# Optimization experiments

Measured on AMD Instinct MI355X. Metric: run time of the kernel, lower is better.

The kernel has to match this reference:

```python
import jax, jax.numpy as jnp
import numpy as np


def _lstm_scan(x_tm, W, b, reset_tm=None):
    """Run an hk.LSTM-equivalent scan over time-major x_tm [L, B, D].

    Gate order i, g, f, o with +1 forget-gate bias (haiku convention).
    If reset_tm [L, B] (bool) is given, state is zeroed BEFORE the step
    whenever reset is True (hk.ResetCore semantics).
    """
    B = x_tm.shape[1]
    H = b.shape[0] // 4

    def step(carry, inp):
        h, c = carry
        if reset_tm is None:
            xt = inp
        else:
            xt, rt = inp
            keep = jnp.logical_not(rt)[:, None]
            h = jnp.where(keep, h, 0.0)
            c = jnp.where(keep, c, 0.0)
        gates = jnp.concatenate([xt, h], axis=-1) @ W + b  # [B, 4H]
        i, g, f, o = jnp.split(gates, 4, axis=-1)
        c = jax.nn.sigmoid(f + 1.0) * c + jax.nn.sigmoid(i) * jnp.tanh(g)
        h = jax.nn.sigmoid(o) * jnp.tanh(c)
        return (h, c), h

    init = (jnp.zeros((B, H), x_tm.dtype), jnp.zeros((B, H), x_tm.dtype))
    xs = x_tm if reset_tm is None else (x_tm, reset_tm)
    _, hs = jax.lax.scan(step, init, xs)
    return hs  # [L, B, H]


def setup_inputs() -> dict:
    key = jax.random.key(0)
    kx, kwf, kwb, kl = jax.random.split(key, 4)
    B, L, D, H = 32, 1024, 512, 512
    scale = 1.0 / np.sqrt(D + H)
    return {
        "x": jax.random.normal(kx, (B, L, D), dtype=jnp.float32),
        "W_fwd": jax.random.normal(kwf, (D + H, 4 * H), dtype=jnp.float32) * scale,
        "b_fwd": jnp.zeros((4 * H,), dtype=jnp.float32),
        "W_bwd": jax.random.normal(kwb, (D + H, 4 * H), dtype=jnp.float32) * scale,
        "b_bwd": jnp.zeros((4 * H,), dtype=jnp.float32),
        "lengths": jax.random.randint(kl, (B,), 1, L + 1),
    }


def reference(x, W_fwd, b_fwd, W_bwd, b_bwd, lengths):
    B, L, D = x.shape
    # reset mask: True for t >= length - 1 (as in original module)
    mask = jnp.arange(L)[None, :] >= lengths[:, None] - 1  # [B, L]

    # forward direction
    h_f = _lstm_scan(jnp.swapaxes(x, 0, 1), W_fwd, b_fwd)  # [L, B, H]
    h_f = jnp.swapaxes(h_f, 0, 1)  # [B, L, H]

    # backward direction: flip time, run ResetCore LSTM, flip back
    x_b = jnp.flip(x, axis=1)
    mask_b = jnp.flip(mask, axis=1)
    h_b = _lstm_scan(jnp.swapaxes(x_b, 0, 1), W_bwd, b_bwd,
                     jnp.swapaxes(mask_b, 0, 1))  # [L, B, H]
    h_b = jnp.flip(jnp.swapaxes(h_b, 0, 1), axis=1)  # [B, L, H]

    return jnp.concatenate([h_f, h_b], axis=-1)  # [B, L, 2H]
```

## Files before the change

### kernel.cpp

```cpp
#include <hip/hip_runtime.h>
#include <stdint.h>


typedef __attribute__((ext_vector_type(8))) short  short8;
typedef __attribute__((ext_vector_type(4))) float  floatx4;

#define LSEQ 1024
#define NB   32
#define DD   512
#define HH   512
#define NG   2048

#define WX_OFF  0ul
#define WH_OFF  (4ul<<20)
#define X_OFF   (8ul<<20)
#define H_OFF   (40ul<<20)
#define RST_OFF ((40ul<<20)+(384ul<<10))
#define TAG_OFF ((40ul<<20)+(388ul<<10))
#define Z_OFF   (41ul<<20)
#define ZF_BYTES (2ul*LSEQ*NB*NG*4)
#define ZB_BYTES (2ul*LSEQ*NB*NG*2)
#define WS_NEED_F32 (Z_OFF + ZF_BYTES)
#define WS_NEED_B16 (Z_OFF + ZB_BYTES)

__device__ inline uint16_t f2bf(float f) {
  uint32_t u = __float_as_uint(f);
  u += 0x7fff + ((u >> 16) & 1);
  return (uint16_t)(u >> 16);
}
__device__ inline float fsigm(float x) { return 1.0f / (1.0f + __expf(-x)); }
__device__ inline float ftanh(float x) { return 1.0f - 2.0f / (__expf(2.0f * x) + 1.0f); }

template <typename ZT> __device__ inline void zstore(ZT* p, float v);
template <> __device__ inline void zstore<float>(float* p, float v) { *p = v; }
template <> __device__ inline void zstore<uint16_t>(uint16_t* p, float v) { *p = f2bf(v); }

template <typename ZT> __device__ inline float2 zld2(const ZT* p);
template <> __device__ inline float2 zld2<float>(const float* p) { return *(const float2*)p; }
template <> __device__ inline float2 zld2<uint16_t>(const uint16_t* p) {
  uint32_t u = *(const uint32_t*)p;
  float2 r;
  r.x = __uint_as_float((u & 0xffffu) << 16);
  r.y = __uint_as_float(u & 0xffff0000u);
  return r;
}

__global__ void k_init(const int* __restrict__ len, uint32_t* __restrict__ rst,
                       int* __restrict__ tags, uint16_t* __restrict__ H)
{
  int tid = blockIdx.x * blockDim.x + threadIdx.x;
  int stride = gridDim.x * blockDim.x;
  for (int i = tid; i < 512; i += stride) tags[i] = 0;
  for (int i = tid; i < 2 * 2 * NB * HH; i += stride) H[i] = 0;
  for (int t = tid; t < LSEQ; t += stride) {
    uint32_t m = 0;
    for (int b = 0; b < NB; ++b)
      m |= ((uint32_t)(t <= LSEQ - len[b])) << b;
    rst[t] = m;
  }
}

__global__ void k_wcast(const float* __restrict__ Wf, const float* __restrict__ Wb,
                        uint16_t* __restrict__ WX, uint16_t* __restrict__ WH)
{
  int tid = blockIdx.x * blockDim.x + threadIdx.x;
  if (tid >= 2 * 1024 * 512) return;
  int dir = tid >> 19;
  int r = tid & ((1 << 19) - 1);
  int k = r >> 9;
  int n4 = (r & 511) * 4;
  const float* W = dir ? Wb : Wf;
  const float4 v = *(const float4*)(W + (size_t)k * NG + n4);
  uint16_t* dst;
  int kk;
  if (k < DD) { dst = WX + (size_t)dir * NG * DD; kk = k; }
  else        { dst = WH + (size_t)dir * NG * HH; kk = k - DD; }
  dst[(size_t)(n4 + 0) * 512 + kk] = f2bf(v.x);
  dst[(size_t)(n4 + 1) * 512 + kk] = f2bf(v.y);
  dst[(size_t)(n4 + 2) * 512 + kk] = f2bf(v.z);
  dst[(size_t)(n4 + 3) * 512 + kk] = f2bf(v.w);
}

__global__ void k_xcast(const float* __restrict__ x, uint16_t* __restrict__ X)
{
  int i4 = blockIdx.x * blockDim.x + threadIdx.x;
  if (i4 >= (NB * LSEQ * DD) / 4) return;
  int d4 = (i4 & 127) * 4;
  int t  = (i4 >> 7) & 1023;
  int b  = i4 >> 17;
  const float4 v = *(const float4*)(x + (size_t)i4 * 4);
  uint32_t lo = (uint32_t)f2bf(v.x) | ((uint32_t)f2bf(v.y) << 16);
  uint32_t hi = (uint32_t)f2bf(v.z) | ((uint32_t)f2bf(v.w) << 16);
  uint2 u; u.x = lo; u.y = hi;
  *(uint2*)(X + ((size_t)t * NB + b) * DD + d4) = u;
}

template <typename ZT>
__global__ __launch_bounds__(256) void k_zgemm(
    const uint16_t* __restrict__ X, const uint16_t* __restrict__ WX,
    const float* __restrict__ bf_, const float* __restrict__ bb_,
    ZT* __restrict__ Z)
{
  __shared__ uint16_t sA[128 * 32];
  __shared__ uint16_t sB[128 * 32];

  const int bid = blockIdx.x;
  const int dir = bid >> 12;
  const int rem = bid & 4095;
  const int mtile = rem >> 4;
  const int ntile = rem & 15;
  const int tid = threadIdx.x;
  const int lane = tid & 63;
  const int w = tid >> 6;
  const int wm = (w >> 1) * 64;
  const int wn = (w & 1) * 64;

  const uint16_t* B = WX + (size_t)dir * NG * 512 + (size_t)(ntile * 128) * 512;
  const float* bias = (dir ? bb_ : bf_) + ntile * 128;

  uint4 ra[2], rb[2];
  auto load_tile = [&](int kk) {
#pragma unroll
    for (int j = 0; j < 2; ++j) {
      int c = tid + 256 * j;
      int row = c >> 2, ko = (c & 3) * 8;
      int grow = mtile * 128 + row;
      int step = grow >> 5, bb = grow & 31;
      int srow = dir ? ((1023 - step) * 32 + bb) : grow;
      ra[j] = *(const uint4*)(X + (size_t)srow * 512 + kk * 32 + ko);
      rb[j] = *(const uint4*)(B + (size_t)row * 512 + kk * 32 + ko);
    }
  };
  auto write_tile = [&]() {
#pragma unroll
    for (int j = 0; j < 2; ++j) {
      int c = tid + 256 * j;
      int row = c >> 2, ko = (c & 3) * 8;
      *(uint4*)(sA + row * 32 + ko) = ra[j];
      *(uint4*)(sB + row * 32 + ko) = rb[j];
    }
  };

  floatx4 acc[4][4];
#pragma unroll
  for (int m = 0; m < 4; ++m)
#pragma unroll
    for (int n = 0; n < 4; ++n)
#pragma unroll
      for (int r = 0; r < 4; ++r) acc[m][n][r] = 0.f;

  load_tile(0);
  for (int kk = 0; kk < 16; ++kk) {
    __syncthreads();
    write_tile();
    __syncthreads();
    if (kk < 15) load_tile(kk + 1);
    short8 af[4], bb8[4];
#pragma unroll
    for (int m = 0; m < 4; ++m)
      af[m] = *(const short8*)(sA + (wm + m * 16 + (lane & 15)) * 32 + (lane >> 4) * 8);
#pragma unroll
    for (int n = 0; n < 4; ++n)
      bb8[n] = *(const short8*)(sB + (wn + n * 16 + (lane & 15)) * 32 + (lane >> 4) * 8);
#pragma unroll
    for (int m = 0; m < 4; ++m)
#pragma unroll
      for (int n = 0; n < 4; ++n)
        acc[m][n] = __builtin_amdgcn_mfma_f32_16x16x32_bf16(af[m], bb8[n], acc[m][n], 0, 0, 0);
  }

  ZT* Zo = Z + ((size_t)dir * 32768 + (size_t)mtile * 128) * 2048 + ntile * 128;
#pragma unroll
  for (int n = 0; n < 4; ++n) {
    int col = wn + n * 16 + (lane & 15);
    float bv = bias[col];
#pragma unroll
    for (int m = 0; m < 4; ++m) {
      int row0 = wm + m * 16 + (lane >> 4) * 4;
#pragma unroll
      for (int r = 0; r < 4; ++r)
        zstore<ZT>(Zo + (size_t)(row0 + r) * 2048 + col, acc[m][n][r] + bv);
    }
  }
}

template <typename ZT>
__global__ __launch_bounds__(512, 2) void k_rec(
    const uint16_t* __restrict__ WH, const ZT* __restrict__ Z,
    const uint32_t* __restrict__ rst, uint16_t* __restrict__ hbuf,
    int* __restrict__ tags, float* __restrict__ out)
{
  __shared__ uint16_t sW[128 * 512];
  __shared__ float sG[NB * 128];

  const int tid = threadIdx.x;
  const int lane = tid & 63;
  const int wid = tid >> 6;
  const int gate = wid & 3;
  const int khalf = wid >> 2;
  const int dir = blockIdx.x >> 4;
  const int p = blockIdx.x & 15;

  const int r0 = lane & 15;
  const int k8 = (lane >> 4) * 8;

  {
    const uint16_t* Wg = WH + (size_t)dir * NG * HH;
    for (int i = tid; i < 8192; i += 512) {
      int lrow = i >> 6;
      int k16  = i & 63;
      int n = (lrow >> 5) * 512 + p * 32 + (lrow & 31);
      uint4 v = *(const uint4*)(Wg + (size_t)n * 512 + k16 * 8);
      int byte = lrow * 1024 + k16 * 16;
      *(uint4*)((char*)sW + (byte ^ ((lrow & 7) << 4))) = v;
    }
  }

  short8 zero8;
#pragma unroll
  for (int i = 0; i < 8; ++i) zero8[i] = 0;

  const int swz = (r0 & 7) << 4;
  const int wrow0 = (gate * 32 + r0) * 1024 + (khalf * 256 + k8) * 2;
  const int wrow1 = wrow0 + 16 * 1024;

  float cst0 = 0.f, cst1 = 0.f;
  const int b_e = tid >> 4;
  const int hc0 = (tid & 15) * 2;

  const ZT* Zb = Z + (size_t)dir * LSEQ * NB * NG + (size_t)b_e * NG + p * 32 + hc0;
  uint16_t* hb = hbuf + dir * 2 * NB * HH;
  int* tg = tags + dir * 256;
  int* myslot = tg + p * 16;

  float2 vzi = zld2<ZT>(Zb);
  float2 vzg = zld2<ZT>(Zb + 512);
  float2 vzf = zld2<ZT>(Zb + 1024);
  float2 vzo = zld2<ZT>(Zb + 1536);

  __syncthreads();

  for (int t = 0; t < LSEQ; ++t) {
    const uint32_t rm = dir ? rst[t] : 0u;

    if (t > 0) {
      if (wid == 0) {
        int guard = 0;
        for (;;) {
          int v = t;
          if (lane < 16)
            v = __hip_atomic_load(tg + lane * 16, __ATOMIC_RELAXED,
                                  __HIP_MEMORY_SCOPE_AGENT);
          if (__all(v >= t)) break;
          __builtin_amdgcn_s_sleep(1);
          if (++guard > (1 << 14)) break;
        }
        if (lane < 16)
          (void)__hip_atomic_load(tg + lane * 16, __ATOMIC_ACQUIRE,
                                  __HIP_MEMORY_SCOPE_AGENT);
      }
      __syncthreads();
    }

    const uint16_t* hA = hb + (t & 1) * NB * HH;
    const bool zr0 = (rm >> r0) & 1;
    const bool zr1 = (rm >> (16 + r0)) & 1;
    const int kof = khalf * 256 + k8;

    floatx4 acc[2][2];
#pragma unroll
    for (int m = 0; m < 2; ++m)
#pragma unroll
      for (int n = 0; n < 2; ++n)
#pragma unroll
        for (int r = 0; r < 4; ++r) acc[m][n][r] = 0.f;

#pragma unroll
    for (int kk = 0; kk < 8; ++kk) {
      short8 a0 = *(const short8*)(hA + (size_t)r0 * HH + kof + kk * 32);
      short8 a1 = *(const short8*)(hA + (size_t)(16 + r0) * HH + kof + kk * 32);
      if (zr0) a0 = zero8;
      if (zr1) a1 = zero8;
      short8 b0 = *(const short8*)((const char*)sW + ((wrow0 + kk * 64) ^ swz));
      short8 b1 = *(const short8*)((const char*)sW + ((wrow1 + kk * 64) ^ swz));
      acc[0][0] = __builtin_amdgcn_mfma_f32_16x16x32_bf16(a0, b0, acc[0][0], 0, 0, 0);
      acc[0][1] = __builtin_amdgcn_mfma_f32_16x16x32_bf16(a0, b1, acc[0][1], 0, 0, 0);
      acc[1][0] = __builtin_amdgcn_mfma_f32_16x16x32_bf16(a1, b0, acc[1][0], 0, 0, 0);
      acc[1][1] = __builtin_amdgcn_mfma_f32_16x16x32_bf16(a1, b1, acc[1][1], 0, 0, 0);
    }

    if (khalf == 0) {
#pragma unroll
      for (int m = 0; m < 2; ++m)
#pragma unroll
        for (int n = 0; n < 2; ++n)
#pragma unroll
          for (int r = 0; r < 4; ++r) {
            int row = m * 16 + (lane >> 4) * 4 + r;
            sG[row * 128 + gate * 32 + n * 16 + r0] = acc[m][n][r];
          }
    }
    __syncthreads();
    if (khalf == 1) {
#pragma unroll
      for (int m = 0; m < 2; ++m)
#pragma unroll
        for (int n = 0; n < 2; ++n)
#pragma unroll
          for (int r = 0; r < 4; ++r) {
            int row = m * 16 + (lane >> 4) * 4 + r;
            sG[row * 128 + gate * 32 + n * 16 + r0] += acc[m][n][r];
          }
    }
    __syncthreads();

    const int gb = b_e * 128;
    const bool cz = (rm >> b_e) & 1;
    float hv0, hv1;
#pragma unroll
    for (int j = 0; j < 2; ++j) {
      int hc = hc0 + j;
      float xi = sG[gb + hc]      + (j ? vzi.y : vzi.x);
      float xg = sG[gb + 32 + hc] + (j ? vzg.y : vzg.x);
      float xf = sG[gb + 64 + hc] + (j ? vzf.y : vzf.x);
      float xo = sG[gb + 96 + hc] + (j ? vzo.y : vzo.x);
      float ii = fsigm(xi);
      float gg = ftanh(xg);
      float ff = fsigm(xf + 1.0f);
      float oo = fsigm(xo);
      float cp = j ? cst1 : cst0;
      if (cz) cp = 0.f;
      float cn = ff * cp + ii * gg;
      if (j) cst1 = cn; else cst0 = cn;
      float hn = oo * ftanh(cn);
      if (j) hv1 = hn; else hv0 = hn;
    }
    uint32_t hpack = (uint32_t)f2bf(hv0) | ((uint32_t)f2bf(hv1) << 16);
    __hip_atomic_store(
        (uint32_t*)(hb + ((t + 1) & 1) * NB * HH + (size_t)b_e * HH + p * 32 + hc0),
        hpack, __ATOMIC_RELAXED, __HIP_MEMORY_SCOPE_AGENT);

    asm volatile("s_waitcnt vmcnt(0)" ::: "memory");
    __syncthreads();
    if (tid == 0)
      __hip_atomic_store(myslot, t + 1, __ATOMIC_RELAXED,
                         __HIP_MEMORY_SCOPE_AGENT);

    if (t + 1 < LSEQ) {
      const ZT* zt = Zb + (size_t)(t + 1) * NB * NG;
      vzi = zld2<ZT>(zt);
      vzg = zld2<ZT>(zt + 512);
      vzf = zld2<ZT>(zt + 1024);
      vzo = zld2<ZT>(zt + 1536);
    }

    const int t_x = dir ? (LSEQ - 1 - t) : t;
    float2 ov; ov.x = hv0; ov.y = hv1;
    *(float2*)(out + ((size_t)b_e * LSEQ + t_x) * 1024 + dir * 512 + p * 32 + hc0) = ov;
  }
}

__global__ void k_report(float* __restrict__ out, int n, float val)
{
  int tid = blockIdx.x * blockDim.x + threadIdx.x;
  int stride = gridDim.x * blockDim.x;
  for (int i = tid; i < n; i += stride) out[i] = val;
}

extern "C" void kernel_launch(void* const* d_in, const int* in_sizes, int n_in,
                              void* d_out, int out_size, void* d_ws, size_t ws_size,
                              hipStream_t stream)
{
  const float* x   = (const float*)d_in[0];
  const float* Wf  = (const float*)d_in[1];
  const float* bf_ = (const float*)d_in[2];
  const float* Wb  = (const float*)d_in[3];
  const float* bb_ = (const float*)d_in[4];
  const int*   len = (const int*)d_in[5];
  float* out = (float*)d_out;
  char* ws = (char*)d_ws;

  const bool f32z = ws_size >= WS_NEED_F32;
  if (!f32z && ws_size < WS_NEED_B16) {
    k_report<<<2048, 256, 0, stream>>>(out, out_size,
                                       200.0f + (float)(ws_size >> 20) * 0.1f);
    return;
  }

  uint16_t* WX  = (uint16_t*)(ws + WX_OFF);
  uint16_t* WHp = (uint16_t*)(ws + WH_OFF);
  uint16_t* X   = (uint16_t*)(ws + X_OFF);
  uint16_t* H   = (uint16_t*)(ws + H_OFF);
  uint32_t* RST = (uint32_t*)(ws + RST_OFF);
  int*      TAG = (int*)(ws + TAG_OFF);

  k_init<<<32, 256, 0, stream>>>(len, RST, TAG, H);
  k_wcast<<<4096, 256, 0, stream>>>(Wf, Wb, WX, WHp);
  k_xcast<<<16384, 256, 0, stream>>>(x, X);

  if (f32z) {
    float* Z = (float*)(ws + Z_OFF);
    k_zgemm<float><<<8192, 256, 0, stream>>>(X, WX, bf_, bb_, Z);
    k_rec<float><<<32, 512, 0, stream>>>(WHp, Z, RST, H, TAG, out);
  } else {
    uint16_t* Z = (uint16_t*)(ws + Z_OFF);
    k_zgemm<uint16_t><<<8192, 256, 0, stream>>>(X, WX, bf_, bb_, Z);
    k_rec<uint16_t><<<32, 512, 0, stream>>>(WHp, Z, RST, H, TAG, out);
  }
}
```

Measured before the change: 7.212 ms.

## Fuse input-projection GEMM into recurrent kernel as producer blocks with ready flags

Merges the separate Z GEMM launch into the recurrent kernel. Blocks 32 and above act as producers that compute Z tiles in mtile order, write them as bf16 with write-through stores, and bump per-tile ready counters. The 32 recurrent blocks poll these counters alongside the existing step tags. The aim is to hide the GEMM behind the serial recurrence. In exchange, Z is now always bf16, which lowers precision compared with the fp32 path used when workspace allowed. Z loads also move into the step after the wait instead of being prefetched, and producers could fall behind or share CUs with the recurrent blocks.

```diff
diff --git a/kernel.cpp b/kernel.cpp
--- a/kernel.cpp
+++ b/kernel.cpp
@@ -17,11 +17,10 @@
 #define H_OFF   (40ul<<20)
 #define RST_OFF ((40ul<<20)+(384ul<<10))
 #define TAG_OFF ((40ul<<20)+(388ul<<10))
+#define ZR_OFF  ((40ul<<20)+(392ul<<10))
 #define Z_OFF   (41ul<<20)
-#define ZF_BYTES (2ul*LSEQ*NB*NG*4)
 #define ZB_BYTES (2ul*LSEQ*NB*NG*2)
-#define WS_NEED_F32 (Z_OFF + ZF_BYTES)
-#define WS_NEED_B16 (Z_OFF + ZB_BYTES)
+#define WS_NEED (Z_OFF + ZB_BYTES)
 
 __device__ inline uint16_t f2bf(float f) {
   uint32_t u = __float_as_uint(f);
@@ -31,13 +30,11 @@
 __device__ inline float fsigm(float x) { return 1.0f / (1.0f + __expf(-x)); }
 __device__ inline float ftanh(float x) { return 1.0f - 2.0f / (__expf(2.0f * x) + 1.0f); }
 
-template <typename ZT> __device__ inline void zstore(ZT* p, float v);
-template <> __device__ inline void zstore<float>(float* p, float v) { *p = v; }
-template <> __device__ inline void zstore<uint16_t>(uint16_t* p, float v) { *p = f2bf(v); }
-
-template <typename ZT> __device__ inline float2 zld2(const ZT* p);
-template <> __device__ inline float2 zld2<float>(const float* p) { return *(const float2*)p; }
-template <> __device__ inline float2 zld2<uint16_t>(const uint16_t* p) {
+__device__ inline void zstore_wt(uint16_t* p, uint32_t v) {
+  asm volatile("global_store_short %0, %1, off sc0 sc1"
+               :: "v"(p), "v"(v) : "memory");
+}
+__device__ inline float2 zld2b(const uint16_t* p) {
   uint32_t u = *(const uint32_t*)p;
   float2 r;
   r.x = __uint_as_float((u & 0xffffu) << 16);
@@ -46,11 +43,13 @@
 }
 
 __global__ void k_init(const int* __restrict__ len, uint32_t* __restrict__ rst,
-                       int* __restrict__ tags, uint16_t* __restrict__ H)
+                       int* __restrict__ tags, int* __restrict__ zr,
+                       uint16_t* __restrict__ H)
 {
   int tid = blockIdx.x * blockDim.x + threadIdx.x;
   int stride = gridDim.x * blockDim.x;
   for (int i = tid; i < 512; i += stride) tags[i] = 0;
+  for (int i = tid; i < 2 * 256 * 16; i += stride) zr[i] = 0;
   for (int i = tid; i < 2 * 2 * NB * HH; i += stride) H[i] = 0;
   for (int t = tid; t < LSEQ; t += stride) {
     uint32_t m = 0;
@@ -95,112 +94,107 @@
   *(uint2*)(X + ((size_t)t * NB + b) * DD + d4) = u;
 }
 
-template <typename ZT>
-__global__ __launch_bounds__(256) void k_zgemm(
-    const uint16_t* __restrict__ X, const uint16_t* __restrict__ WX,
+__global__ __launch_bounds__(512, 2) void k_rec(
+    const uint16_t* __restrict__ WH, const uint16_t* __restrict__ WX,
+    const uint16_t* __restrict__ X, uint16_t* __restrict__ Z,
     const float* __restrict__ bf_, const float* __restrict__ bb_,
-    ZT* __restrict__ Z)
-{
-  __shared__ uint16_t sA[128 * 32];
-  __shared__ uint16_t sB[128 * 32];
-
-  const int bid = blockIdx.x;
-  const int dir = bid >> 12;
-  const int rem = bid & 4095;
-  const int mtile = rem >> 4;
-  const int ntile = rem & 15;
-  const int tid = threadIdx.x;
-  const int lane = tid & 63;
-  const int w = tid >> 6;
-  const int wm = (w >> 1) * 64;
-  const int wn = (w & 1) * 64;
-
-  const uint16_t* B = WX + (size_t)dir * NG * 512 + (size_t)(ntile * 128) * 512;
-  const float* bias = (dir ? bb_ : bf_) + ntile * 128;
-
-  uint4 ra[2], rb[2];
-  auto load_tile = [&](int kk) {
-#pragma unroll
-    for (int j = 0; j < 2; ++j) {
-      int c = tid + 256 * j;
-      int row = c >> 2, ko = (c & 3) * 8;
-      int grow = mtile * 128 + row;
-      int step = grow >> 5, bb = grow & 31;
-      int srow = dir ? ((1023 - step) * 32 + bb) : grow;
-      ra[j] = *(const uint4*)(X + (size_t)srow * 512 + kk * 32 + ko);
-      rb[j] = *(const uint4*)(B + (size_t)row * 512 + kk * 32 + ko);
-    }
-  };
-  auto write_tile = [&]() {
-#pragma unroll
-    for (int j = 0; j < 2; ++j) {
-      int c = tid + 256 * j;
-      int row = c >> 2, ko = (c & 3) * 8;
-      *(uint4*)(sA + row * 32 + ko) = ra[j];
-      *(uint4*)(sB + row * 32 + ko) = rb[j];
-    }
-  };
-
-  floatx4 acc[4][4];
-#pragma unroll
-  for (int m = 0; m < 4; ++m)
-#pragma unroll
-    for (int n = 0; n < 4; ++n)
-#pragma unroll
-      for (int r = 0; r < 4; ++r) acc[m][n][r] = 0.f;
-
-  load_tile(0);
-  for (int kk = 0; kk < 16; ++kk) {
-    __syncthreads();
-    write_tile();
-    __syncthreads();
-    if (kk < 15) load_tile(kk + 1);
-    short8 af[4], bb8[4];
-#pragma unroll
-    for (int m = 0; m < 4; ++m)
-      af[m] = *(const short8*)(sA + (wm + m * 16 + (lane & 15)) * 32 + (lane >> 4) * 8);
-#pragma unroll
-    for (int n = 0; n < 4; ++n)
-      bb8[n] = *(const short8*)(sB + (wn + n * 16 + (lane & 15)) * 32 + (lane >> 4) * 8);
-#pragma unroll
-    for (int m = 0; m < 4; ++m)
-#pragma unroll
-      for (int n = 0; n < 4; ++n)
-        acc[m][n] = __builtin_amdgcn_mfma_f32_16x16x32_bf16(af[m], bb8[n], acc[m][n], 0, 0, 0);
-  }
-
-  ZT* Zo = Z + ((size_t)dir * 32768 + (size_t)mtile * 128) * 2048 + ntile * 128;
-#pragma unroll
-  for (int n = 0; n < 4; ++n) {
-    int col = wn + n * 16 + (lane & 15);
-    float bv = bias[col];
-#pragma unroll
-    for (int m = 0; m < 4; ++m) {
-      int row0 = wm + m * 16 + (lane >> 4) * 4;
-#pragma unroll
-      for (int r = 0; r < 4; ++r)
-        zstore<ZT>(Zo + (size_t)(row0 + r) * 2048 + col, acc[m][n][r] + bv);
-    }
-  }
-}
-
-template <typename ZT>
-__global__ __launch_bounds__(512, 2) void k_rec(
-    const uint16_t* __restrict__ WH, const ZT* __restrict__ Z,
     const uint32_t* __restrict__ rst, uint16_t* __restrict__ hbuf,
-    int* __restrict__ tags, float* __restrict__ out)
+    int* __restrict__ tags, int* __restrict__ zready,
+    float* __restrict__ out)
 {
   __shared__ uint16_t sW[128 * 512];
   __shared__ float sG[NB * 128];
 
+  const int bid = blockIdx.x;
   const int tid = threadIdx.x;
   const int lane = tid & 63;
   const int wid = tid >> 6;
+
+  if (bid >= 32) {
+    uint16_t* sA = sW;
+    uint16_t* sB = sW + 128 * 32;
+    const int wm = (wid >> 2) * 64;
+    const int wn = (wid & 3) * 32;
+
+    for (int tau = bid - 32; tau < 8192; tau += 224) {
+      const int mtile = tau >> 5;
+      const int rem = tau & 31;
+      const int dir = rem >> 4;
+      const int ntile = rem & 15;
+
+      const uint16_t* B = WX + (size_t)dir * NG * 512 + (size_t)(ntile * 128) * 512;
+      const float* bias = (dir ? bb_ : bf_) + ntile * 128;
+
+      uint4 ra, rb;
+      auto load_tile = [&](int kk) {
+        int row = tid >> 2, ko = (tid & 3) * 8;
+        int grow = mtile * 128 + row;
+        int step = grow >> 5, bb = grow & 31;
+        int srow = dir ? ((1023 - step) * 32 + bb) : grow;
+        ra = *(const uint4*)(X + (size_t)srow * 512 + kk * 32 + ko);
+        rb = *(const uint4*)(B + (size_t)row * 512 + kk * 32 + ko);
+      };
+      auto write_tile = [&]() {
+        int row = tid >> 2, ko = (tid & 3) * 8;
+        *(uint4*)(sA + row * 32 + ko) = ra;
+        *(uint4*)(sB + row * 32 + ko) = rb;
+      };
+
+      floatx4 acc[4][2];
+#pragma unroll
+      for (int m = 0; m < 4; ++m)
+#pragma unroll
+        for (int n = 0; n < 2; ++n)
+#pragma unroll
+          for (int r = 0; r < 4; ++r) acc[m][n][r] = 0.f;
+
+      load_tile(0);
+      for (int kk = 0; kk < 16; ++kk) {
+        __syncthreads();
+        write_tile();
+        __syncthreads();
+        if (kk < 15) load_tile(kk + 1);
+        short8 af[4], bb8[2];
+#pragma unroll
+        for (int m = 0; m < 4; ++m)
+          af[m] = *(const short8*)(sA + (wm + m * 16 + (lane & 15)) * 32 + (lane >> 4) * 8);
+#pragma unroll
+        for (int n = 0; n < 2; ++n)
+          bb8[n] = *(const short8*)(sB + (wn + n * 16 + (lane & 15)) * 32 + (lane >> 4) * 8);
+#pragma unroll
+        for (int m = 0; m < 4; ++m)
+#pragma unroll
+          for (int n = 0; n < 2; ++n)
+            acc[m][n] = __builtin_amdgcn_mfma_f32_16x16x32_bf16(af[m], bb8[n], acc[m][n], 0, 0, 0);
+      }
+
+      uint16_t* Zo = Z + ((size_t)dir * 32768 + (size_t)mtile * 128) * 2048 + ntile * 128;
+#pragma unroll
+      for (int n = 0; n < 2; ++n) {
+        int col = wn + n * 16 + (lane & 15);
+        float bv = bias[col];
+#pragma unroll
+        for (int m = 0; m < 4; ++m) {
+          int row0 = wm + m * 16 + (lane >> 4) * 4;
+#pragma unroll
+          for (int r = 0; r < 4; ++r)
+            zstore_wt(Zo + (size_t)(row0 + r) * 2048 + col,
+                      (uint32_t)f2bf(acc[m][n][r] + bv));
+        }
+      }
+      asm volatile("s_waitcnt vmcnt(0)" ::: "memory");
+      __syncthreads();
+      if (tid == 0)
+        __hip_atomic_fetch_add(zready + ((size_t)dir * 256 + mtile) * 16, 1,
+                               __ATOMIC_RELAXED, __HIP_MEMORY_SCOPE_AGENT);
+    }
+    return;
+  }
+
   const int gate = wid & 3;
   const int khalf = wid >> 2;
-  const int dir = blockIdx.x >> 4;
-  const int p = blockIdx.x & 15;
-
+  const int dir = bid >> 4;
+  const int p = bid & 15;
   const int r0 = lane & 15;
   const int k8 = (lane >> 4) * 8;
 
@@ -228,39 +222,43 @@
   const int b_e = tid >> 4;
   const int hc0 = (tid & 15) * 2;
 
-  const ZT* Zb = Z + (size_t)dir * LSEQ * NB * NG + (size_t)b_e * NG + p * 32 + hc0;
+  const uint16_t* Zb = Z + (size_t)dir * LSEQ * NB * NG + (size_t)b_e * NG + p * 32 + hc0;
   uint16_t* hb = hbuf + dir * 2 * NB * HH;
   int* tg = tags + dir * 256;
   int* myslot = tg + p * 16;
-
-  float2 vzi = zld2<ZT>(Zb);
-  float2 vzg = zld2<ZT>(Zb + 512);
-  float2 vzf = zld2<ZT>(Zb + 1024);
-  float2 vzo = zld2<ZT>(Zb + 1536);
+  const int* zrd = zready + (size_t)dir * 256 * 16;
 
   __syncthreads();
 
   for (int t = 0; t < LSEQ; ++t) {
     const uint32_t rm = dir ? rst[t] : 0u;
 
-    if (t > 0) {
-      if (wid == 0) {
-        int guard = 0;
-        for (;;) {
-          int v = t;
-          if (lane < 16)
-            v = __hip_atomic_load(tg + lane * 16, __ATOMIC_RELAXED,
-                                  __HIP_MEMORY_SCOPE_AGENT);
-          if (__all(v >= t)) break;
-          __builtin_amdgcn_s_sleep(1);
-          if (++guard > (1 << 14)) break;
-        }
+    if (wid == 0) {
+      const int mt = t >> 2;
+      int guard = 0;
+      for (;;) {
+        int ok = 1;
         if (lane < 16)
-          (void)__hip_atomic_load(tg + lane * 16, __ATOMIC_ACQUIRE,
-                                  __HIP_MEMORY_SCOPE_AGENT);
+          ok = __hip_atomic_load(tg + lane * 16, __ATOMIC_RELAXED,
+                                 __HIP_MEMORY_SCOPE_AGENT) >= t;
+        else if (lane == 16)
+          ok = __hip_atomic_load(zrd + mt * 16, __ATOMIC_RELAXED,
+                                 __HIP_MEMORY_SCOPE_AGENT) >= 16;
+        if (__all(ok)) break;
+        __builtin_amdgcn_s_sleep(1);
+        if (++guard > (1 << 15)) break;
       }
-      __syncthreads();
-    }
+      if (lane < 16)
+        (void)__hip_atomic_load(tg + lane * 16, __ATOMIC_ACQUIRE,
+                                __HIP_MEMORY_SCOPE_AGENT);
+    }
+    __syncthreads();
+
+    const uint16_t* zt = Zb + (size_t)t * NB * NG;
+    float2 vzi = zld2b(zt);
+    float2 vzg = zld2b(zt + 512);
+    float2 vzf = zld2b(zt + 1024);
+    float2 vzo = zld2b(zt + 1536);
 
     const uint16_t* hA = hb + (t & 1) * NB * HH;
     const bool zr0 = (rm >> r0) & 1;
@@ -346,14 +344,6 @@
       __hip_atomic_store(myslot, t + 1, __ATOMIC_RELAXED,
                          __HIP_MEMORY_SCOPE_AGENT);
 
-    if (t + 1 < LSEQ) {
-      const ZT* zt = Zb + (size_t)(t + 1) * NB * NG;
-      vzi = zld2<ZT>(zt);
-      vzg = zld2<ZT>(zt + 512);
-      vzf = zld2<ZT>(zt + 1024);
-      vzo = zld2<ZT>(zt + 1536);
-    }
-
     const int t_x = dir ? (LSEQ - 1 - t) : t;
     float2 ov; ov.x = hv0; ov.y = hv1;
     *(float2*)(out + ((size_t)b_e * LSEQ + t_x) * 1024 + dir * 512 + p * 32 + hc0) = ov;
@@ -380,8 +370,7 @@
   float* out = (float*)d_out;
   char* ws = (char*)d_ws;
 
-  const bool f32z = ws_size >= WS_NEED_F32;
-  if (!f32z && ws_size < WS_NEED_B16) {
+  if (ws_size < WS_NEED) {
     k_report<<<2048, 256, 0, stream>>>(out, out_size,
                                        200.0f + (float)(ws_size >> 20) * 0.1f);
     return;
@@ -393,18 +382,11 @@
   uint16_t* H   = (uint16_t*)(ws + H_OFF);
   uint32_t* RST = (uint32_t*)(ws + RST_OFF);
   int*      TAG = (int*)(ws + TAG_OFF);
-
-  k_init<<<32, 256, 0, stream>>>(len, RST, TAG, H);
+  int*      ZR  = (int*)(ws + ZR_OFF);
+  uint16_t* Z   = (uint16_t*)(ws + Z_OFF);
+
+  k_init<<<64, 256, 0, stream>>>(len, RST, TAG, ZR, H);
   k_wcast<<<4096, 256, 0, stream>>>(Wf, Wb, WX, WHp);
   k_xcast<<<16384, 256, 0, stream>>>(x, X);
-
-  if (f32z) {
-    float* Z = (float*)(ws + Z_OFF);
-    k_zgemm<float><<<8192, 256, 0, stream>>>(X, WX, bf_, bb_, Z);
-    k_rec<float><<<32, 512, 0, stream>>>(WHp, Z, RST, H, TAG, out);
-  } else {
-    uint16_t* Z = (uint16_t*)(ws + Z_OFF);
-    k_zgemm<uint16_t><<<8192, 256, 0, stream>>>(X, WX, bf_, bb_, Z);
-    k_rec<uint16_t><<<32, 512, 0, stream>>>(WHp, Z, RST, H, TAG, out);
-  }
-}
+  k_rec<<<256, 512, 0, stream>>>(WHp, WX, X, Z, bf_, bb_, RST, H, TAG, ZR, out);
+}
```

Result: faster. 6.581 ms, median of 2 (-8.7%).
